# Performance work log

Measured on AMD Instinct MI355X. Metric: run time of the kernel, lower is better.

## Reference

```python
import jax, jax.numpy as jnp
import numpy as np
from jax import lax

TEMP = 0.1
EPS_LOG = 1e-6
RMS_EPS = 1e-6
K_NEIGHBORS = 8


def setup_inputs() -> dict:
    key = jax.random.key(0)
    ks = jax.random.split(key, 8)
    B, T, D = 2, 2048, 1024
    N, DK, DM = 32768, 256, 256
    return {
        "x": jax.random.normal(ks[0], (B, T, D), dtype=jnp.float32),
        "keys": jax.random.normal(ks[1], (N, DK), dtype=jnp.float32),
        "vals": jax.random.normal(ks[2], (N, DM), dtype=jnp.float32),
        "W_in": jax.random.normal(ks[3], (DK, D), dtype=jnp.float32) / np.sqrt(D),
        "b_in": jnp.zeros((DK,), dtype=jnp.float32),
        "W_out": jax.random.normal(ks[4], (D, K_NEIGHBORS * DM), dtype=jnp.float32) / np.sqrt(K_NEIGHBORS * DM),
        "b_out": jnp.zeros((D,), dtype=jnp.float32),
        "rms_w": jnp.ones((D,), dtype=jnp.float32),
    }


def _memory_forward(x, keys, vals, W_in, b_in, W_out, b_out, rms_w):
    B, T, D = x.shape
    N, DM = vals.shape
    # proj_in: [B,T,D] -> [B,T,DK]
    q = jnp.einsum("btd,kd->btk", x, W_in) + b_in
    # squared euclidean distances to memory keys: [B,T,N]
    q2 = jnp.sum(q * q, axis=-1, keepdims=True)          # [B,T,1]
    k2 = jnp.sum(keys * keys, axis=-1)                   # [N]
    qk = jnp.einsum("btc,nc->btn", q, keys)              # [B,T,N]
    logits = -(q2 - 2.0 * qk + k2) / TEMP                # [B,T,N]

    # N3Net-style continuous k-NN: k rounds of softmax selection
    def step(lg, _):
        w = jax.nn.softmax(lg, axis=-1)                  # [B,T,N]
        out = jnp.einsum("btn,nf->btf", w, vals)         # [B,T,DM]
        lg = lg + jnp.log1p(-w + EPS_LOG)
        return lg, out

    _, outs = lax.scan(step, logits, None, length=K_NEIGHBORS)  # [K,B,T,DM]
    nearest = jnp.moveaxis(outs, 0, 2).reshape(B, T, K_NEIGHBORS * DM)

    out = jnp.einsum("btf,df->btd", nearest, W_out) + b_out
    # RMSNorm
    var = jnp.mean(out.astype(jnp.float32) ** 2, axis=-1, keepdims=True)
    out = out * lax.rsqrt(var + RMS_EPS)
    return rms_w * out


def reference(x, keys, vals, W_in, b_in, W_out, b_out, rms_w):
    return _memory_forward(x, keys, vals, W_in, b_in, W_out, b_out, rms_w)
```

## Files before the change

### kernel.cpp

```cpp
#include <hip/hip_runtime.h>
#include <hip/hip_bf16.h>

#define ROWS  4096
#define DDIM  1024
#define DKDIM 256
#define NKEYS 32768
#define DMDIM 256
#define KN    8
#define FDIM  2048
#define CAPS  1536
#define SURV  128
#define SURV2 96
#define MARGIN   16.0f
#define REFILT_M 12.25f
#define EXACT_M  109.0f

typedef float  f32x4  __attribute__((ext_vector_type(4)));
typedef __bf16 bf16x8 __attribute__((ext_vector_type(8)));

static __device__ __forceinline__ unsigned enc_f32(float f) {
  unsigned u = __float_as_uint(f);
  return u ^ ((unsigned)((int)u >> 31) | 0x80000000u);
}
static __device__ __forceinline__ float dec_f32(unsigned u) {
  unsigned b = (u & 0x80000000u) ? (u ^ 0x80000000u) : ~u;
  return __uint_as_float(b);
}
static __device__ __forceinline__ unsigned short f2bf(float f) {
  unsigned u = __float_as_uint(f);
  u += 0x7FFFu + ((u >> 16) & 1u);
  return (unsigned short)(u >> 16);
}
static __device__ __forceinline__ unsigned pack_cand(float s, int n) {
  float q = (s + 1024.f) * 64.f;
  int u = (int)q;
  u = u < 0 ? 0 : (u > 131071 ? 131071 : u);
  return ((unsigned)u << 15) | (unsigned)n;
}
static __device__ __forceinline__ float cand_score(unsigned p) {
  return (float)(p >> 15) * (1.f / 64.f) - 1024.f;
}
static __device__ __forceinline__ void gld16(const void* g, void* l) {
  __builtin_amdgcn_global_load_lds((const __attribute__((address_space(1))) void*)g,
                                   (__attribute__((address_space(3))) void*)l, 16, 0, 0);
}

__global__ __launch_bounds__(256) void prep_all(const float* __restrict__ keys,
                                                const float* __restrict__ Wout,
                                                unsigned short* __restrict__ kbf,
                                                float* __restrict__ k2,
                                                unsigned short* __restrict__ wbf,
                                                unsigned* __restrict__ rowmax) {
  const int b = blockIdx.x, t = threadIdx.x;
  if (b < 8192) {
    const int row = b * 4 + (t >> 6);
    const int ln  = t & 63;
    const float4 v = *(const float4*)(keys + (size_t)row * DKDIM + ln * 4);
    ushort4 o;
    o.x = f2bf(v.x); o.y = f2bf(v.y); o.z = f2bf(v.z); o.w = f2bf(v.w);
    *(ushort4*)(kbf + (size_t)row * DKDIM + ln * 4) = o;
    float ss = v.x*v.x + v.y*v.y + v.z*v.z + v.w*v.w;
    for (int off = 32; off; off >>= 1) ss += __shfl_down(ss, off);
    if (ln == 0) k2[row] = ss;
  } else if (b < 10240) {
    const int i = (b - 8192) * 256 + t;
    const float4 v = *(const float4*)(Wout + (size_t)i * 4);
    ushort4 o;
    o.x = f2bf(v.x); o.y = f2bf(v.y); o.z = f2bf(v.z); o.w = f2bf(v.w);
    *(ushort4*)(wbf + (size_t)i * 4) = o;
  } else {
    rowmax[(b - 10240) * 256 + t] = 0u;
  }
}

__global__ __launch_bounds__(256) void qproj(const float* __restrict__ x,
                                             const float* __restrict__ Win,
                                             const float* __restrict__ bin,
                                             float* __restrict__ qf,
                                             unsigned short* __restrict__ qbf) {
  __shared__ __align__(16) float As[64][68];
  __shared__ __align__(16) float Bs[64][68];
  const int bm = blockIdx.x, bn = blockIdx.y;
  const int t  = threadIdx.x;
  const int tx = t & 15, ty = t >> 4;
  float acc[4][4] = {};
  for (int ks = 0; ks < 16; ++ks) {
    __syncthreads();
    for (int l = t; l < 1024; l += 256) {
      const int row = l >> 4, kc = l & 15;
      *(float4*)(&As[row][kc * 4]) =
          *(const float4*)(x + (size_t)(bm * 64 + row) * DDIM + ks * 64 + kc * 4);
      *(float4*)(&Bs[row][kc * 4]) =
          *(const float4*)(Win + (size_t)(bn * 64 + row) * DDIM + ks * 64 + kc * 4);
    }
    __syncthreads();
    for (int kk = 0; kk < 64; kk += 4) {
      float4 av[4], bv[4];
#pragma unroll
      for (int i = 0; i < 4; ++i) av[i] = *(const float4*)(&As[ty * 4 + i][kk]);
#pragma unroll
      for (int j = 0; j < 4; ++j) bv[j] = *(const float4*)(&Bs[tx * 4 + j][kk]);
#pragma unroll
      for (int i = 0; i < 4; ++i)
#pragma unroll
        for (int j = 0; j < 4; ++j)
          acc[i][j] += av[i].x * bv[j].x + av[i].y * bv[j].y +
                       av[i].z * bv[j].z + av[i].w * bv[j].w;
    }
  }
#pragma unroll
  for (int i = 0; i < 4; ++i)
#pragma unroll
    for (int j = 0; j < 4; ++j) {
      const int m = bm * 64 + ty * 4 + i, n = bn * 64 + tx * 4 + j;
      const float q = acc[i][j] + bin[n];
      qf[(size_t)m * DKDIM + n] = q;
      qbf[(size_t)m * DKDIM + n] = f2bf(q);
    }
}

template <int KD>
static __device__ __forceinline__ void gemm_tile(const unsigned short* __restrict__ A,
                                                 const unsigned short* __restrict__ B,
                                                 int bm, int bn,
                                                 unsigned short* As, unsigned short* Bs,
                                                 f32x4 acc[4][4]) {
  const int tid  = threadIdx.x;
  const int lane = tid & 63, wave = tid >> 6;
  const int quad = lane >> 4, l15 = lane & 15;
  const int wr = (wave >> 1) * 64, wc = (wave & 1) * 64;
  const int srow = tid >> 2;
  const int scg  = (tid & 3) ^ ((srow >> 1) & 3);
  const int qa   = quad ^ ((l15 >> 1) & 3);
  const unsigned short* gA = A + (size_t)(bm * 128 + srow) * KD + scg * 8;
  const unsigned short* gB = B + (size_t)(bn * 128 + srow) * KD + scg * 8;
  for (int ks = 0; ks < KD / 32; ++ks) {
    __syncthreads();
    gld16(gA + ks * 32,                     As + tid * 8);
    gld16(gA + (size_t)64 * KD + ks * 32,   As + 2048 + tid * 8);
    gld16(gB + ks * 32,                     Bs + tid * 8);
    gld16(gB + (size_t)64 * KD + ks * 32,   Bs + 2048 + tid * 8);
    __syncthreads();
    bf16x8 af[4], bfr[4];
#pragma unroll
    for (int i = 0; i < 4; ++i)
      af[i] = *(const bf16x8*)(As + (wr + i * 16 + l15) * 32 + qa * 8);
#pragma unroll
    for (int j = 0; j < 4; ++j)
      bfr[j] = *(const bf16x8*)(Bs + (wc + j * 16 + l15) * 32 + qa * 8);
#pragma unroll
    for (int i = 0; i < 4; ++i)
#pragma unroll
      for (int j = 0; j < 4; ++j)
        acc[i][j] = __builtin_amdgcn_mfma_f32_16x16x32_bf16(af[i], bfr[j], acc[i][j], 0, 0, 0);
  }
}

__global__ __launch_bounds__(256) void score_select(const unsigned short* __restrict__ qbf,
                                                    const unsigned short* __restrict__ kbf,
                                                    const float* __restrict__ k2,
                                                    unsigned* __restrict__ rowmax,
                                                    int* __restrict__ cnt,
                                                    unsigned* __restrict__ cand) {
  __shared__ __align__(16) unsigned short As[4096];
  __shared__ __align__(16) unsigned short Bs[4096];
  __shared__ float wm[128][2];
  __shared__ float thr[128];
  f32x4 acc[4][4] = {};
  gemm_tile<DKDIM>(qbf, kbf, blockIdx.x, blockIdx.y, As, Bs, acc);
  const int t = threadIdx.x;
  const int lane = t & 63, wave = t >> 6;
  const int quad = lane >> 4, l15 = lane & 15;
  const int wr = (wave >> 1) * 64, wc = (wave & 1) * 64;
  float k2v[4];
#pragma unroll
  for (int j = 0; j < 4; ++j) k2v[j] = k2[blockIdx.y * 128 + wc + j * 16 + l15];
#pragma unroll
  for (int i = 0; i < 4; ++i)
#pragma unroll
    for (int r = 0; r < 4; ++r) {
      float v = -3.4e38f;
#pragma unroll
      for (int j = 0; j < 4; ++j) v = fmaxf(v, 2.f * acc[i][j][r] - k2v[j]);
      for (int m = 8; m; m >>= 1) v = fmaxf(v, __shfl_xor(v, m));
      if (l15 == 0) wm[wr + i * 16 + quad * 4 + r][wave & 1] = v;
    }
  __syncthreads();
  if (t < 128) {
    const float tile = fmaxf(wm[t][0], wm[t][1]);
    const unsigned old = atomicMax(&rowmax[blockIdx.x * 128 + t], enc_f32(tile));
    thr[t] = fmaxf(tile, dec_f32(old)) - MARGIN;
  }
  __syncthreads();
#pragma unroll
  for (int i = 0; i < 4; ++i)
#pragma unroll
    for (int r = 0; r < 4; ++r) {
      const int rl = wr + i * 16 + quad * 4 + r;
      const float th = thr[rl];
      const int gm = blockIdx.x * 128 + rl;
#pragma unroll
      for (int j = 0; j < 4; ++j) {
        const float s = 2.f * acc[i][j][r] - k2v[j];
        if (s >= th) {
          const int n = blockIdx.y * 128 + wc + j * 16 + l15;
          const int pos = atomicAdd(&cnt[gm], 1);
          if (pos < CAPS) cand[(size_t)gm * CAPS + pos] = pack_cand(s, n);
        }
      }
    }
}

__global__ __launch_bounds__(256) void knn_rounds(const float* __restrict__ qf,
                                                  const float* __restrict__ keys,
                                                  const float* __restrict__ k2,
                                                  const float* __restrict__ vals,
                                                  const int* __restrict__ cnt,
                                                  const unsigned* __restrict__ cand,
                                                  unsigned short* __restrict__ nearest) {
  __shared__ __align__(16) float qs[DKDIM];
  __shared__ unsigned cl[CAPS];
  __shared__ float red[256];
  __shared__ int   sidx[SURV];
  __shared__ float Ls[SURV];
  __shared__ int   sidx2[SURV2];
  __shared__ float L2v[SURV2];
  __shared__ float cs[SURV2];
  __shared__ float Ws[SURV2 * KN];
  __shared__ int n1, n2;
  const int row = blockIdx.x, t = threadIdx.x;
  const int C = min(cnt[row], CAPS);
  qs[t] = qf[(size_t)row * DKDIM + t];
  if (t == 0) { n1 = 0; n2 = 0; }
  float m = -3.4e38f;
  for (int i = t; i < C; i += 256) {
    const unsigned p = cand[(size_t)row * CAPS + i];
    cl[i] = p;
    m = fmaxf(m, cand_score(p));
  }
  red[t] = m;
  __syncthreads();
  for (int s = 128; s; s >>= 1) {
    if (t < s) red[t] = fmaxf(red[t], red[t + s]);
    __syncthreads();
  }
  const float th1 = red[0] - REFILT_M;
  for (int i = t; i < C; i += 256) {
    if (cand_score(cl[i]) >= th1) {
      const int p = atomicAdd(&n1, 1);
      if (p < SURV) sidx[p] = (int)(cl[i] & 32767u);
    }
  }
  if (t < SURV2) cs[t] = 0.f;
  __syncthreads();
  const int S1 = min(n1, SURV);
  const int wv = t >> 6, ln = t & 63;
  for (int i = wv; i < S1; i += 4) {
    const int n = sidx[i];
    const float4 kv = *(const float4*)(keys + (size_t)n * DKDIM + ln * 4);
    const float4 qv = *(const float4*)(qs + ln * 4);
    float d = kv.x * qv.x + kv.y * qv.y + kv.z * qv.z + kv.w * qv.w;
    for (int o = 32; o; o >>= 1) d += __shfl_down(d, o);
    if (ln == 0) Ls[i] = (2.f * d - k2[n]) / 0.1f;
  }
  __syncthreads();
  red[t] = (t < S1) ? Ls[t] : -3.4e38f;
  __syncthreads();
  for (int s = 128; s; s >>= 1) {
    if (t < s) red[t] = fmaxf(red[t], red[t + s]);
    __syncthreads();
  }
  const float Lmax = red[0];
  if (t < S1 && Ls[t] >= Lmax - EXACT_M) {
    const int p = atomicAdd(&n2, 1);
    if (p < SURV2) { sidx2[p] = sidx[t]; L2v[p] = Ls[t]; }
  }
  __syncthreads();
  const int S2 = min(n2, SURV2);
  if (t < 64) {
    for (int j = 0; j < KN; ++j) {
      float lm = -3.4e38f;
      for (int i = t; i < S2; i += 64) lm = fmaxf(lm, L2v[i] + cs[i]);
      for (int o = 32; o; o >>= 1) lm = fmaxf(lm, __shfl_xor(lm, o));
      float zs = 0.f;
      for (int i = t; i < S2; i += 64) {
        const float e = expf(L2v[i] + cs[i] - lm);
        Ws[i * KN + j] = e; zs += e;
      }
      for (int o = 32; o; o >>= 1) zs += __shfl_xor(zs, o);
      const float Zi = 1.f / zs;
      for (int i = t; i < S2; i += 64) {
        const float w = Ws[i * KN + j] * Zi;
        Ws[i * KN + j] = w;
        cs[i] += log1pf(1e-6f - w);
      }
    }
  }
  __syncthreads();
  float acc[KN] = {};
  for (int i = 0; i < S2; ++i) {
    const float v = vals[(size_t)sidx2[i] * DMDIM + t];
#pragma unroll
    for (int j = 0; j < KN; ++j) acc[j] += Ws[i * KN + j] * v;
  }
#pragma unroll
  for (int j = 0; j < KN; ++j)
    nearest[(size_t)row * FDIM + j * DMDIM + t] = f2bf(acc[j]);
}

__global__ __launch_bounds__(256) void out_gemm(const unsigned short* __restrict__ nbf,
                                                const unsigned short* __restrict__ wbf,
                                                const float* __restrict__ bout,
                                                float* __restrict__ out) {
  __shared__ __align__(16) unsigned short As[4096];
  __shared__ __align__(16) unsigned short Bs[4096];
  f32x4 acc[4][4] = {};
  gemm_tile<FDIM>(nbf, wbf, blockIdx.x, blockIdx.y, As, Bs, acc);
  const int lane = threadIdx.x & 63, wave = threadIdx.x >> 6;
  const int quad = lane >> 4, l15 = lane & 15;
  const int wr = (wave >> 1) * 64, wc = (wave & 1) * 64;
#pragma unroll
  for (int i = 0; i < 4; ++i)
#pragma unroll
    for (int r = 0; r < 4; ++r) {
      const int gm = blockIdx.x * 128 + wr + i * 16 + quad * 4 + r;
#pragma unroll
      for (int j = 0; j < 4; ++j) {
        const int n = blockIdx.y * 128 + wc + j * 16 + l15;
        out[(size_t)gm * DDIM + n] = acc[i][j][r] + bout[n];
      }
    }
}

__global__ __launch_bounds__(256) void rmsnorm(float* __restrict__ out,
                                               const float* __restrict__ rmsw) {
  __shared__ float red[256];
  const int row = blockIdx.x, t = threadIdx.x;
  const float4 v = *(const float4*)(out + (size_t)row * DDIM + t * 4);
  red[t] = v.x * v.x + v.y * v.y + v.z * v.z + v.w * v.w;
  __syncthreads();
  for (int s = 128; s; s >>= 1) {
    if (t < s) red[t] += red[t + s];
    __syncthreads();
  }
  const float scale = rsqrtf(red[0] / (float)DDIM + 1e-6f);
  const float4 w = *(const float4*)(rmsw + t * 4);
  float4 o;
  o.x = v.x * scale * w.x; o.y = v.y * scale * w.y;
  o.z = v.z * scale * w.z; o.w = v.w * scale * w.w;
  *(float4*)(out + (size_t)row * DDIM + t * 4) = o;
}

extern "C" void kernel_launch(void* const* d_in, const int* in_sizes, int n_in,
                              void* d_out, int out_size, void* d_ws, size_t ws_size,
                              hipStream_t stream) {
  const float* x    = (const float*)d_in[0];
  const float* keys = (const float*)d_in[1];
  const float* vals = (const float*)d_in[2];
  const float* Win  = (const float*)d_in[3];
  const float* bin  = (const float*)d_in[4];
  const float* Wout = (const float*)d_in[5];
  const float* bout = (const float*)d_in[6];
  const float* rmsw = (const float*)d_in[7];
  float* out = (float*)d_out;
  char* ws = (char*)d_ws;

  float*          q_f32   = (float*)(ws);
  unsigned short* q_bf    = (unsigned short*)(ws + 4194304);
  unsigned short* k_bf    = (unsigned short*)(ws + 6291456);
  unsigned short* nearest = (unsigned short*)(ws + 6291456);
  float*          k2      = (float*)(ws + 23068672);
  unsigned*       rowmax  = (unsigned*)(ws + 23199744);
  int*            cnt     = (int*)(ws + 23216128);
  unsigned*       cand    = (unsigned*)(ws + 23232512);
  unsigned short* w_bf    = (unsigned short*)(ws + 48398336);

  prep_all<<<10272, 256, 0, stream>>>(keys, Wout, k_bf, k2, w_bf, rowmax);
  qproj<<<dim3(ROWS / 64, DKDIM / 64), 256, 0, stream>>>(x, Win, bin, q_f32, q_bf);
  score_select<<<dim3(ROWS / 128, NKEYS / 128), 256, 0, stream>>>(q_bf, k_bf, k2, rowmax, cnt, cand);
  knn_rounds<<<ROWS, 256, 0, stream>>>(q_f32, keys, k2, vals, cnt, cand, nearest);
  out_gemm<<<dim3(ROWS / 128, DDIM / 128), 256, 0, stream>>>(nearest, w_bf, bout, out);
  rmsnorm<<<ROWS, 256, 0, stream>>>(out, rmsw);
}
```

Before: 430.5 us.

## Make score_select persistent over key chunks with per-slot LDS candidate counters

The score/select kernel now runs on a grid of 8x32 blocks instead of one block per 128x128 tile. Each block keeps its full 128-row query tile in LDS and walks 32 key tiles from a 4096-key chunk, prefetching the next key tile during candidate emission. It keeps a running row max, so the selection threshold tightens as it scans. Candidates go to per-(row, chunk) slots counted by LDS atomics rather than global atomics, and knn_rounds concatenates the eight slots. The risks are only 4 waves per CU with about 128KB of LDS, less latency hiding, and a per-slot cap that can drop candidates.

```diff
diff --git a/kernel.cpp b/kernel.cpp
--- a/kernel.cpp
+++ b/kernel.cpp
@@ -9,6 +9,7 @@
 #define KN    8
 #define FDIM  2048
 #define CAPS  1536
+#define SLOT  184
 #define SURV  128
 #define SURV2 96
 #define MARGIN   16.0f
@@ -162,53 +163,116 @@
                                                     unsigned* __restrict__ rowmax,
                                                     int* __restrict__ cnt,
                                                     unsigned* __restrict__ cand) {
-  __shared__ __align__(16) unsigned short As[4096];
-  __shared__ __align__(16) unsigned short Bs[4096];
+  __shared__ __align__(16) unsigned short As[8 * 4096];
+  __shared__ __align__(16) unsigned short Bs[8 * 4096];
   __shared__ float wm[128][2];
   __shared__ float thr[128];
-  f32x4 acc[4][4] = {};
-  gemm_tile<DKDIM>(qbf, kbf, blockIdx.x, blockIdx.y, As, Bs, acc);
+  __shared__ int   pcnt[128];
+  const int cg = blockIdx.x, bm = blockIdx.y;
   const int t = threadIdx.x;
   const int lane = t & 63, wave = t >> 6;
   const int quad = lane >> 4, l15 = lane & 15;
   const int wr = (wave >> 1) * 64, wc = (wave & 1) * 64;
-  float k2v[4];
-#pragma unroll
-  for (int j = 0; j < 4; ++j) k2v[j] = k2[blockIdx.y * 128 + wc + j * 16 + l15];
-#pragma unroll
-  for (int i = 0; i < 4; ++i)
-#pragma unroll
-    for (int r = 0; r < 4; ++r) {
-      float v = -3.4e38f;
-#pragma unroll
-      for (int j = 0; j < 4; ++j) v = fmaxf(v, 2.f * acc[i][j][r] - k2v[j]);
-      for (int m = 8; m; m >>= 1) v = fmaxf(v, __shfl_xor(v, m));
-      if (l15 == 0) wm[wr + i * 16 + quad * 4 + r][wave & 1] = v;
-    }
-  __syncthreads();
-  if (t < 128) {
-    const float tile = fmaxf(wm[t][0], wm[t][1]);
-    const unsigned old = atomicMax(&rowmax[blockIdx.x * 128 + t], enc_f32(tile));
-    thr[t] = fmaxf(tile, dec_f32(old)) - MARGIN;
-  }
-  __syncthreads();
-#pragma unroll
-  for (int i = 0; i < 4; ++i)
-#pragma unroll
-    for (int r = 0; r < 4; ++r) {
-      const int rl = wr + i * 16 + quad * 4 + r;
-      const float th = thr[rl];
-      const int gm = blockIdx.x * 128 + rl;
-#pragma unroll
-      for (int j = 0; j < 4; ++j) {
-        const float s = 2.f * acc[i][j][r] - k2v[j];
-        if (s >= th) {
-          const int n = blockIdx.y * 128 + wc + j * 16 + l15;
-          const int pos = atomicAdd(&cnt[gm], 1);
-          if (pos < CAPS) cand[(size_t)gm * CAPS + pos] = pack_cand(s, n);
+  const int srow = t >> 2;
+  const int scg  = (t & 3) ^ ((srow >> 1) & 3);
+  const int qa   = quad ^ ((l15 >> 1) & 3);
+
+  if (t < 128) pcnt[t] = 0;
+
+  {
+    const unsigned short* gA = qbf + (size_t)(bm * 128 + srow) * DKDIM + scg * 8;
+#pragma unroll
+    for (int ks = 0; ks < 8; ++ks) {
+      gld16(gA + ks * 32,                      As + ks * 4096 + t * 8);
+      gld16(gA + (size_t)64 * DKDIM + ks * 32, As + ks * 4096 + 2048 + t * 8);
+    }
+    const unsigned short* gB = kbf + ((size_t)cg * 4096 + srow) * DKDIM + scg * 8;
+#pragma unroll
+    for (int ks = 0; ks < 8; ++ks) {
+      gld16(gB + ks * 32,                      Bs + ks * 4096 + t * 8);
+      gld16(gB + (size_t)64 * DKDIM + ks * 32, Bs + ks * 4096 + 2048 + t * 8);
+    }
+  }
+
+  float lmax = -3.4e38f;
+  f32x4 acc[4][4] = {};
+  for (int tile = 0; tile < 32; ++tile) {
+    __syncthreads();
+#pragma unroll
+    for (int ks = 0; ks < 8; ++ks) {
+      bf16x8 af[4], bv[4];
+#pragma unroll
+      for (int i = 0; i < 4; ++i)
+        af[i] = *(const bf16x8*)(As + ks * 4096 + (wr + i * 16 + l15) * 32 + qa * 8);
+#pragma unroll
+      for (int j = 0; j < 4; ++j)
+        bv[j] = *(const bf16x8*)(Bs + ks * 4096 + (wc + j * 16 + l15) * 32 + qa * 8);
+#pragma unroll
+      for (int i = 0; i < 4; ++i)
+#pragma unroll
+        for (int j = 0; j < 4; ++j)
+          acc[i][j] = __builtin_amdgcn_mfma_f32_16x16x32_bf16(af[i], bv[j], acc[i][j], 0, 0, 0);
+    }
+    float k2v[4];
+#pragma unroll
+    for (int j = 0; j < 4; ++j) k2v[j] = k2[cg * 4096 + tile * 128 + wc + j * 16 + l15];
+#pragma unroll
+    for (int i = 0; i < 4; ++i)
+#pragma unroll
+      for (int r = 0; r < 4; ++r) {
+        float v = -3.4e38f;
+#pragma unroll
+        for (int j = 0; j < 4; ++j) v = fmaxf(v, 2.f * acc[i][j][r] - k2v[j]);
+        for (int m = 8; m; m >>= 1) v = fmaxf(v, __shfl_xor(v, m));
+        if (l15 == 0) wm[wr + i * 16 + quad * 4 + r][wave & 1] = v;
+      }
+    __syncthreads();
+    if (t < 128) {
+      const float tmax = fmaxf(wm[t][0], wm[t][1]);
+      lmax = fmaxf(lmax, tmax);
+      const unsigned old = atomicMax(&rowmax[bm * 128 + t], enc_f32(lmax));
+      thr[t] = fmaxf(lmax, dec_f32(old)) - MARGIN;
+    }
+    __syncthreads();
+    float th[16];
+#pragma unroll
+    for (int i = 0; i < 4; ++i)
+#pragma unroll
+      for (int r = 0; r < 4; ++r)
+        th[i * 4 + r] = thr[wr + i * 16 + quad * 4 + r];
+    if (tile + 1 < 32) {
+      const unsigned short* gB = kbf + ((size_t)cg * 4096 + (size_t)(tile + 1) * 128 + srow) * DKDIM + scg * 8;
+#pragma unroll
+      for (int ks = 0; ks < 8; ++ks) {
+        gld16(gB + ks * 32,                      Bs + ks * 4096 + t * 8);
+        gld16(gB + (size_t)64 * DKDIM + ks * 32, Bs + ks * 4096 + 2048 + t * 8);
+      }
+    }
+#pragma unroll
+    for (int i = 0; i < 4; ++i)
+#pragma unroll
+      for (int r = 0; r < 4; ++r) {
+        const int rl = wr + i * 16 + quad * 4 + r;
+#pragma unroll
+        for (int j = 0; j < 4; ++j) {
+          const float s = 2.f * acc[i][j][r] - k2v[j];
+          if (s >= th[i * 4 + r]) {
+            const int n = cg * 4096 + tile * 128 + wc + j * 16 + l15;
+            const int pos = atomicAdd(&pcnt[rl], 1);
+            if (pos < SLOT)
+              cand[((size_t)(bm * 128 + rl) * 8 + cg) * SLOT + pos] = pack_cand(s, n);
+          }
         }
       }
-    }
+#pragma unroll
+    for (int i = 0; i < 4; ++i)
+#pragma unroll
+      for (int j = 0; j < 4; ++j)
+#pragma unroll
+        for (int r2 = 0; r2 < 4; ++r2) acc[i][j][r2] = 0.f;
+  }
+  __syncthreads();
+  if (t < 128) cnt[(size_t)(bm * 128 + t) * 8 + cg] = min(pcnt[t], SLOT);
 }
 
 __global__ __launch_bounds__(256) void knn_rounds(const float* __restrict__ qf,
@@ -229,14 +293,19 @@
   __shared__ float Ws[SURV2 * KN];
   __shared__ int n1, n2;
   const int row = blockIdx.x, t = threadIdx.x;
-  const int C = min(cnt[row], CAPS);
   qs[t] = qf[(size_t)row * DKDIM + t];
   if (t == 0) { n1 = 0; n2 = 0; }
   float m = -3.4e38f;
-  for (int i = t; i < C; i += 256) {
-    const unsigned p = cand[(size_t)row * CAPS + i];
-    cl[i] = p;
-    m = fmaxf(m, cand_score(p));
+  int C = 0;
+  for (int s8 = 0; s8 < 8; ++s8) {
+    const int Cs = min(cnt[(size_t)row * 8 + s8], SLOT);
+    const unsigned* cp = cand + ((size_t)row * 8 + s8) * SLOT;
+    for (int i = t; i < Cs; i += 256) {
+      const unsigned p = cp[i];
+      cl[C + i] = p;
+      m = fmaxf(m, cand_score(p));
+    }
+    C += Cs;
   }
   red[t] = m;
   __syncthreads();
@@ -372,12 +441,12 @@
   float*          k2      = (float*)(ws + 23068672);
   unsigned*       rowmax  = (unsigned*)(ws + 23199744);
   int*            cnt     = (int*)(ws + 23216128);
-  unsigned*       cand    = (unsigned*)(ws + 23232512);
-  unsigned short* w_bf    = (unsigned short*)(ws + 48398336);
-
-  prep_all<<<10272, 256, 0, stream>>>(keys, Wout, k_bf, k2, w_bf, rowmax);
+  unsigned*       cand    = (unsigned*)(ws + 23347200);
+  unsigned short* w_bf    = (unsigned short*)(ws + 47464448);
+
+  prep_all<<<10256, 256, 0, stream>>>(keys, Wout, k_bf, k2, w_bf, rowmax);
   qproj<<<dim3(ROWS / 64, DKDIM / 64), 256, 0, stream>>>(x, Win, bin, q_f32, q_bf);
-  score_select<<<dim3(ROWS / 128, NKEYS / 128), 256, 0, stream>>>(q_bf, k_bf, k2, rowmax, cnt, cand);
+  score_select<<<dim3(8, 32), 256, 0, stream>>>(q_bf, k_bf, k2, rowmax, cnt, cand);
   knn_rounds<<<ROWS, 256, 0, stream>>>(q_f32, keys, k2, vals, cnt, cand, nearest);
   out_gemm<<<dim3(ROWS / 128, DDIM / 128), 256, 0, stream>>>(nearest, w_bf, bout, out);
   rmsnorm<<<ROWS, 256, 0, stream>>>(out, rmsw);
```

After: 529.7 us. +23.0%, slower.
